# Performance work log

Hardware: AMD Instinct MI355X
Metric: run time of the kernel (lower is better)

The kernel has to match this reference:

```python
import jax, jax.numpy as jnp
import numpy as np

D_MODEL = 1024
D_STATE = 16
D_CONV = 4
EXPAND = 2
D_INNER = D_MODEL * EXPAND


def setup_inputs() -> dict:
    key = jax.random.key(0)
    ks = jax.random.split(key, 10)
    B, L = 2, 2048
    x = jax.random.normal(ks[0], (B, L, D_MODEL), jnp.float32)
    W_in = jax.random.normal(ks[1], (2 * D_INNER, D_MODEL), jnp.float32) * (1.0 / np.sqrt(D_MODEL))
    conv_w = jax.random.normal(ks[2], (D_INNER, 1, D_CONV), jnp.float32) * (1.0 / np.sqrt(D_CONV))
    conv_b = jax.random.normal(ks[3], (D_INNER,), jnp.float32) * 0.1
    W_x = jax.random.normal(ks[4], (2 * D_STATE + 1, D_INNER), jnp.float32) * (1.0 / np.sqrt(D_INNER))
    A_log = jnp.log(jnp.abs(jax.random.normal(ks[5], (D_INNER, D_STATE), jnp.float32)) + 1e-4)
    D_param = jnp.ones((D_INNER,), jnp.float32)
    W_dt = jax.random.normal(ks[6], (D_INNER, 1), jnp.float32)
    b_dt = jax.random.normal(ks[7], (D_INNER,), jnp.float32) * 0.1
    W_out = jax.random.normal(ks[8], (D_MODEL, D_INNER), jnp.float32) * (1.0 / np.sqrt(D_INNER))
    return {"x": x, "W_in": W_in, "conv_w": conv_w, "conv_b": conv_b, "W_x": W_x,
            "A_log": A_log, "D_param": D_param, "W_dt": W_dt, "b_dt": b_dt, "W_out": W_out}


def _forward(x, W_in, conv_w, conv_b, W_x, A_log, D_param, W_dt, b_dt, W_out):
    B, L, _ = x.shape
    xz = x @ W_in.T                                  # [B,L,2*d_inner]
    x_ssm, z = jnp.split(xz, 2, axis=-1)
    # causal depthwise conv: torch pads both sides d_conv-1 then truncates to L == left-pad only
    xc = jnp.transpose(x_ssm, (0, 2, 1))             # [B,d_inner,L]
    xc = jax.lax.conv_general_dilated(
        xc, conv_w, window_strides=(1,), padding=[(D_CONV - 1, 0)],
        feature_group_count=D_INNER, dimension_numbers=("NCH", "OIH", "NCH"))
    xc = xc + conv_b[None, :, None]
    x_ssm = jax.nn.silu(jnp.transpose(xc, (0, 2, 1)))  # [B,L,d_inner]
    proj = x_ssm @ W_x.T                              # [B,L,2*d_state+1]
    B_ssm = proj[..., :D_STATE]                       # [B,L,d_state]
    C_ssm = proj[..., D_STATE:2 * D_STATE]            # [B,L,d_state]
    dt = jax.nn.softplus(proj[..., -1:] * W_dt[:, 0] + b_dt)  # [B,L,d_inner]
    A = -jnp.exp(A_log)                               # [d_inner,d_state]

    def step(h, inp):
        dt_t, Bt, Ct, xt = inp                        # [B,d_inner],[B,n],[B,n],[B,d_inner]
        dA = jnp.exp(dt_t[..., None] * A)             # [B,d_inner,d_state]
        h = dA * h + (xt * dt_t)[..., None] * Bt[:, None, :]
        y = jnp.einsum("bdn,bn->bd", h, Ct)
        return h, y

    h0 = jnp.zeros((B, D_INNER, D_STATE), x.dtype)
    inputs = (jnp.transpose(dt, (1, 0, 2)), jnp.transpose(B_ssm, (1, 0, 2)),
              jnp.transpose(C_ssm, (1, 0, 2)), jnp.transpose(x_ssm, (1, 0, 2)))
    _, ys = jax.lax.scan(step, h0, inputs)            # ys: [L,B,d_inner]
    y = jnp.transpose(ys, (1, 0, 2)) + x_ssm * D_param
    y = y * jax.nn.silu(z)
    return y @ W_out.T


def reference(x, W_in, conv_w, conv_b, W_x, A_log, D_param, W_dt, b_dt, W_out):
    return _forward(x, W_in, conv_w, conv_b, W_x, A_log, D_param, W_dt, b_dt, W_out)
```

## Files before the change

kernel.cpp:

```cpp
#include <hip/hip_runtime.h>
#include <hip/hip_bf16.h>
#include <cstddef>

#define DMODEL 1024
#define DI     2048
#define DS     16
#define LSEQ   2048
#define BATCH  2
#define NC     128
#define TCH    (LSEQ / NC)

typedef __attribute__((ext_vector_type(8))) short short8;
typedef __attribute__((ext_vector_type(4))) float f32x4;
typedef __attribute__((ext_vector_type(2))) float f32x2;
typedef __attribute__((ext_vector_type(8))) unsigned short us8;

__device__ __forceinline__ unsigned short f2bf(float f) {
    unsigned int u = __float_as_uint(f);
    unsigned int r = (u + 0x7fff + ((u >> 16) & 1)) >> 16;
    return (unsigned short)r;
}
__device__ __forceinline__ float bf2f(unsigned short b) {
    return __uint_as_float(((unsigned int)b) << 16);
}

__device__ __forceinline__ float fexp2(float x) {
#if __has_builtin(__builtin_amdgcn_exp2f)
    return __builtin_amdgcn_exp2f(x);
#else
    return exp2f(x);
#endif
}
__device__ __forceinline__ float flog2(float x) {
#if __has_builtin(__builtin_amdgcn_logf)
    return __builtin_amdgcn_logf(x);
#else
    return log2f(x);
#endif
}

#define LOG2E 1.4426950408889634f
#define RLOG2E 0.6931471805599453f

__device__ __forceinline__ float softplus_f(float v) {
    return (v > 20.f) ? v : flog2(1.f + fexp2(v * LOG2E)) * RLOG2E;
}

__device__ __forceinline__ void gload_lds16(const void* g, void* l) {
    __builtin_amdgcn_global_load_lds(
        (const __attribute__((address_space(1))) unsigned int*)g,
        (__attribute__((address_space(3))) unsigned int*)l, 16, 0, 0);
}

__device__ __forceinline__ void cvt8_store(const float* __restrict__ in,
                                           unsigned short* __restrict__ out, int i) {
    const float4* p = reinterpret_cast<const float4*>(in) + (size_t)i * 2;
    float4 v0 = p[0], v1 = p[1];
    us8 o;
    o[0] = f2bf(v0.x); o[1] = f2bf(v0.y); o[2] = f2bf(v0.z); o[3] = f2bf(v0.w);
    o[4] = f2bf(v1.x); o[5] = f2bf(v1.y); o[6] = f2bf(v1.z); o[7] = f2bf(v1.w);
    *reinterpret_cast<us8*>(out + (size_t)i * 8) = o;
}

#define PREP_X   524288
#define PREP_WI  (PREP_X + 524288)
#define PREP_WO  (PREP_WI + 262144)
#define PREP_WX  (PREP_WO + 12288)
#define PREP_A   (PREP_WX + 32768)
__global__ void prep_all(const float* __restrict__ x, const float* __restrict__ W_in,
                         const float* __restrict__ W_out, const float* __restrict__ wx,
                         const float* __restrict__ A_log,
                         unsigned short* __restrict__ Xb, unsigned short* __restrict__ W_inb,
                         unsigned short* __restrict__ W_outb, unsigned short* __restrict__ Wxb48,
                         float* __restrict__ At2) {
    int i = blockIdx.x * 256 + threadIdx.x;
    if (i < PREP_X) {
        cvt8_store(x, Xb, i);
    } else if (i < PREP_WI) {
        cvt8_store(W_in, W_inb, i - PREP_X);
    } else if (i < PREP_WO) {
        cvt8_store(W_out, W_outb, i - PREP_WI);
    } else if (i < PREP_WX) {
        int j = i - PREP_WO;
        size_t o = (size_t)j * 8;
        int row = (int)(o >> 11);
        if (row < 33) cvt8_store(wx, Wxb48, j);
        else *reinterpret_cast<us8*>(Wxb48 + o) = (us8)0;
    } else if (i < PREP_A) {
        int j = i - PREP_WX;
        int n = j / DI, d = j % DI;
        At2[j] = -__expf(A_log[d * DS + n]) * LOG2E;
    }
}

#define NTK1 32
__global__ __launch_bounds__(512, 4)
void gemm1_2b(const unsigned short* __restrict__ A, const unsigned short* __restrict__ B,
              unsigned short* __restrict__ C) {
    __shared__ unsigned short As[2][128 * 32];
    __shared__ unsigned short Bs[2][256 * 32];

    const int tid = threadIdx.x;
    const int wid = tid >> 6, ln = tid & 63;
    const int wm = wid >> 2, wn = wid & 3;

    int wg = blockIdx.x;
    wg = (wg & 7) * 64 + (wg >> 3);
    const int m0 = (wg >> 4) * 128;
    const int n0 = (wg & 15) * 256;

    const int srow = tid >> 2;
    const int sun  = tid & 3;
    const int ksrc = ((sun ^ ((srow >> 1) & 3)) * 8);

    const int fr = ln & 15;
    const int fku = (ln >> 4);

    f32x4 acc[4][4] = {};

    #define STAGE1(kt, c)                                                                  \
        do {                                                                               \
            gload_lds16(A + (size_t)(m0 + srow) * 1024 + (kt) * 32 + ksrc,                 \
                        &As[c][srow * 32 + sun * 8]);                                      \
            gload_lds16(B + (size_t)(n0 + srow) * 1024 + (kt) * 32 + ksrc,                 \
                        &Bs[c][srow * 32 + sun * 8]);                                      \
            gload_lds16(B + (size_t)(n0 + 128 + srow) * 1024 + (kt) * 32 + ksrc,           \
                        &Bs[c][(128 + srow) * 32 + sun * 8]);                              \
        } while (0)

    STAGE1(0, 0);
    asm volatile("s_waitcnt vmcnt(0)" ::: "memory");
    __builtin_amdgcn_s_barrier();
    __builtin_amdgcn_sched_barrier(0);

    for (int kt = 0; kt < NTK1; ++kt) {
        const int c = kt & 1;
        if (kt + 1 < NTK1) STAGE1(kt + 1, c ^ 1);

        short8 af[4], bfr[4];
        #pragma unroll
        for (int i = 0; i < 4; ++i) {
            int r = wm * 64 + i * 16 + fr;
            int u = fku ^ ((r >> 1) & 3);
            af[i] = *reinterpret_cast<const short8*>(&As[c][r * 32 + u * 8]);
        }
        #pragma unroll
        for (int j = 0; j < 4; ++j) {
            int r = wn * 64 + j * 16 + fr;
            int u = fku ^ ((r >> 1) & 3);
            bfr[j] = *reinterpret_cast<const short8*>(&Bs[c][r * 32 + u * 8]);
        }
        __builtin_amdgcn_sched_barrier(0);
        __builtin_amdgcn_s_setprio(1);
        #pragma unroll
        for (int i = 0; i < 4; ++i)
            #pragma unroll
            for (int j = 0; j < 4; ++j)
                acc[i][j] = __builtin_amdgcn_mfma_f32_16x16x32_bf16(af[i], bfr[j], acc[i][j], 0, 0, 0);
        __builtin_amdgcn_s_setprio(0);
        __builtin_amdgcn_sched_barrier(0);

        if (kt + 1 < NTK1) asm volatile("s_waitcnt vmcnt(0)" ::: "memory");
        __builtin_amdgcn_s_barrier();
        __builtin_amdgcn_sched_barrier(0);
    }
    #undef STAGE1

    const int cr = (ln >> 4) * 4, cc = ln & 15;
    #pragma unroll
    for (int i = 0; i < 4; ++i) {
        int row = m0 + wm * 64 + i * 16 + cr;
        #pragma unroll
        for (int j = 0; j < 4; ++j) {
            int col = n0 + wn * 64 + j * 16 + cc;
            #pragma unroll
            for (int r = 0; r < 4; ++r)
                C[(size_t)(row + r) * 4096 + col] = f2bf(acc[i][j][r]);
        }
    }
}

#define NT3 64
__global__ __launch_bounds__(256, 2)
void gemm3_pipe(const unsigned short* __restrict__ A,
                const unsigned short* __restrict__ B,
                float* __restrict__ C) {
    __shared__ unsigned short As[4][128 * 32];
    __shared__ unsigned short Bs[4][64 * 32];

    const int tid = threadIdx.x;
    const int wid = tid >> 6, ln = tid & 63;
    const int wm = wid >> 1, wn = wid & 1;

    int wg = blockIdx.x;
    wg = (wg & 7) * 64 + (wg >> 3);
    const int m0 = (wg >> 4) * 128;
    const int n0 = (wg & 15) * 64;

    const int srow = tid >> 2;
    const int sun  = tid & 3;
    const int ksrc = ((sun ^ ((srow >> 1) & 3)) * 8);

    const int fr = ln & 15;
    const int fku = (ln >> 4);

    f32x4 acc[4][2] = {};

    #define STAGE3(kt)                                                                     \
        do {                                                                               \
            const int bq_ = (kt) & 3;                                                      \
            gload_lds16(A + (size_t)(m0 + srow) * 2048 + (kt) * 32 + ksrc,                 \
                        &As[bq_][srow * 32 + sun * 8]);                                    \
            gload_lds16(A + (size_t)(m0 + 64 + srow) * 2048 + (kt) * 32 + ksrc,            \
                        &As[bq_][(64 + srow) * 32 + sun * 8]);                             \
            gload_lds16(B + (size_t)(n0 + srow) * 2048 + (kt) * 32 + ksrc,                 \
                        &Bs[bq_][srow * 32 + sun * 8]);                                    \
        } while (0)

    STAGE3(0); STAGE3(1); STAGE3(2);
    asm volatile("s_waitcnt vmcnt(6)" ::: "memory");
    __builtin_amdgcn_s_barrier();
    __builtin_amdgcn_sched_barrier(0);

    for (int kt = 0; kt < NT3; ++kt) {
        const int bq = kt & 3;
        if (kt + 3 < NT3) STAGE3(kt + 3);

        short8 af[4], bfr[2];
        #pragma unroll
        for (int i = 0; i < 4; ++i) {
            int r = wm * 64 + i * 16 + fr;
            int u = fku ^ ((r >> 1) & 3);
            af[i] = *reinterpret_cast<const short8*>(&As[bq][r * 32 + u * 8]);
        }
        #pragma unroll
        for (int j = 0; j < 2; ++j) {
            int r = wn * 32 + j * 16 + fr;
            int u = fku ^ ((r >> 1) & 3);
            bfr[j] = *reinterpret_cast<const short8*>(&Bs[bq][r * 32 + u * 8]);
        }
        __builtin_amdgcn_sched_barrier(0);
        __builtin_amdgcn_s_setprio(1);
        #pragma unroll
        for (int i = 0; i < 4; ++i)
            #pragma unroll
            for (int j = 0; j < 2; ++j)
                acc[i][j] = __builtin_amdgcn_mfma_f32_16x16x32_bf16(af[i], bfr[j], acc[i][j], 0, 0, 0);
        __builtin_amdgcn_s_setprio(0);
        __builtin_amdgcn_sched_barrier(0);

        if (kt < NT3 - 3)       asm volatile("s_waitcnt vmcnt(6)" ::: "memory");
        else if (kt == NT3 - 3) asm volatile("s_waitcnt vmcnt(3)" ::: "memory");
        else if (kt == NT3 - 2) asm volatile("s_waitcnt vmcnt(0)" ::: "memory");
        __builtin_amdgcn_s_barrier();
        __builtin_amdgcn_sched_barrier(0);
    }
    #undef STAGE3

    const int cr = (ln >> 4) * 4, cc = ln & 15;
    #pragma unroll
    for (int i = 0; i < 4; ++i) {
        int row = m0 + wm * 64 + i * 16 + cr;
        #pragma unroll
        for (int j = 0; j < 2; ++j) {
            int col = n0 + wn * 32 + j * 16 + cc;
            #pragma unroll
            for (int r = 0; r < 4; ++r)
                C[(size_t)(row + r) * 1024 + col] = acc[i][j][r];
        }
    }
}

__global__ void conv_silu(const unsigned short* __restrict__ xzb, const float* __restrict__ cw,
                          const float* __restrict__ cb, unsigned short* __restrict__ xactb) {
    int i = blockIdx.x * 256 + threadIdx.x;
    if (i >= BATCH * LSEQ * DI / 8) return;
    int d0 = (i % (DI / 8)) * 8;
    int l  = (i / (DI / 8)) % LSEQ;
    int b  = i / ((DI / 8) * LSEQ);

    float4 w[8];
    #pragma unroll
    for (int j = 0; j < 8; ++j)
        w[j] = *reinterpret_cast<const float4*>(cw + (d0 + j) * 4);

    float acc[8];
    #pragma unroll
    for (int j = 0; j < 8; ++j) acc[j] = cb[d0 + j];

    #pragma unroll
    for (int t = 0; t < 4; ++t) {
        int ls = l - 3 + t;
        if (ls >= 0) {
            us8 v = *reinterpret_cast<const us8*>(xzb + (size_t)(b * LSEQ + ls) * 4096 + d0);
            #pragma unroll
            for (int j = 0; j < 8; ++j) {
                float wt = (t == 0) ? w[j].x : (t == 1) ? w[j].y : (t == 2) ? w[j].z : w[j].w;
                acc[j] += bf2f(v[j]) * wt;
            }
        }
    }
    us8 o;
    #pragma unroll
    for (int j = 0; j < 8; ++j) {
        float v = acc[j] / (1.f + __expf(-acc[j]));
        o[j] = f2bf(v);
    }
    *reinterpret_cast<us8*>(xactb + (size_t)i * 8) = o;
}

__global__ __launch_bounds__(256)
void gemm_proj_mfma(const unsigned short* __restrict__ Xb, const unsigned short* __restrict__ Wxb,
                    float* __restrict__ projp) {
    __shared__ unsigned short As[64 * 32];
    __shared__ unsigned short Bs[48 * 32];

    const int tid = threadIdx.x;
    const int wv = tid >> 6, ln = tid & 63;
    const int m0 = blockIdx.x * 64;
    const int kz = blockIdx.y;
    const int srow = tid >> 2, skoff = (tid & 3) * 8;
    const int fr = ln & 15, fk = (ln >> 4) * 8;

    f32x4 acc[3] = {};

    const int k0base = kz * 512;
    for (int k0 = k0base; k0 < k0base + 512; k0 += 32) {
        gload_lds16(Xb + (size_t)(m0 + srow) * DI + k0 + skoff, &As[wv * 512]);
        if (wv < 3)
            gload_lds16(Wxb + (size_t)srow * DI + k0 + skoff, &Bs[wv * 512]);
        __syncthreads();

        short8 af = *reinterpret_cast<const short8*>(&As[(wv * 16 + fr) * 32 + fk]);
        #pragma unroll
        for (int j = 0; j < 3; ++j) {
            short8 bf_ = *reinterpret_cast<const short8*>(&Bs[(j * 16 + fr) * 32 + fk]);
            acc[j] = __builtin_amdgcn_mfma_f32_16x16x32_bf16(af, bf_, acc[j], 0, 0, 0);
        }
        __syncthreads();
    }

    const int cr = (ln >> 4) * 4, cc = ln & 15;
    #pragma unroll
    for (int j = 0; j < 3; ++j) {
        int col = j * 16 + cc;
        if (col < 33) {
            #pragma unroll
            for (int r = 0; r < 4; ++r) {
                int row = m0 + wv * 16 + cr + r;
                projp[(size_t)row * 144 + kz * 36 + col] = acc[j][r];
            }
        }
    }
}

__global__ void proj_combine(const float* __restrict__ projp, float* __restrict__ proj) {
    int idx = blockIdx.x * 256 + threadIdx.x;
    if (idx >= BATCH * LSEQ * 33) return;
    int row = idx / 33, col = idx % 33;
    float s = 0.f;
    #pragma unroll
    for (int kz = 0; kz < 4; ++kz)
        s += projp[(size_t)row * 144 + kz * 36 + col];
    proj[(size_t)row * 36 + col] = s;
}

__global__ __launch_bounds__(256)
void scan_phase1(const unsigned short* __restrict__ xactb, const float* __restrict__ proj,
                 const float* __restrict__ At2, const float* __restrict__ W_dt,
                 const float* __restrict__ b_dt, const float* __restrict__ Dp,
                 unsigned short* __restrict__ Hend,
                 float* __restrict__ dtsum, unsigned short* __restrict__ yloc) {
    const int d = blockIdx.x * 256 + threadIdx.x;
    const int c = blockIdx.y;
    const int b = blockIdx.z;

    f32x2 A2[DS / 2], h2[DS / 2];
    #pragma unroll
    for (int p = 0; p < DS / 2; ++p) {
        A2[p] = (f32x2){At2[(2 * p) * DI + d], At2[(2 * p + 1) * DI + d]};
        h2[p] = (f32x2){0.f, 0.f};
    }
    const float wdt = W_dt[d], bdt = b_dt[d], Dv = Dp[d];
    float ssum = 0.f;

    const int l0 = c * TCH;
    #pragma unroll 2
    for (int l = l0; l < l0 + TCH; ++l) {
        const size_t row = (size_t)(b * LSEQ + l);
        const float* pr = proj + row * 36;
        float dt = softplus_f(pr[32] * wdt + bdt);
        ssum += dt;
        float x = bf2f(xactb[row * DI + d]);
        float xdt = x * dt;
        f32x2 xdt2 = (f32x2){xdt, xdt};
        f32x2 y2 = (f32x2){0.f, 0.f};
        #pragma unroll
        for (int p = 0; p < DS / 2; ++p) {
            f32x2 t = A2[p] * dt;
            f32x2 e2 = (f32x2){fexp2(t.x), fexp2(t.y)};
            h2[p] = e2 * h2[p] + xdt2 * (f32x2){pr[2 * p], pr[2 * p + 1]};
            y2 += h2[p] * (f32x2){pr[16 + 2 * p], pr[17 + 2 * p]};
        }
        yloc[row * DI + d] = f2bf(y2.x + y2.y + x * Dv);
    }
    size_t base = ((size_t)(b * NC + c) * DS) * DI + d;
    #pragma unroll
    for (int p = 0; p < DS / 2; ++p) {
        Hend[base + (size_t)(2 * p) * DI]     = f2bf(h2[p].x);
        Hend[base + (size_t)(2 * p + 1) * DI] = f2bf(h2[p].y);
    }
    dtsum[(size_t)(b * NC + c) * DI + d] = ssum;
}

__global__ void scan_phase2(unsigned short* __restrict__ H, const float* __restrict__ dtsum,
                            const float* __restrict__ At2) {
    int idx = blockIdx.x * 256 + threadIdx.x;
    int b = idx / (DS * DI);
    int r = idx % (DS * DI);
    int n = r / DI, d = r % DI;
    float A2 = At2[n * DI + d];
    float h = 0.f;
    #pragma unroll 4
    for (int c = 0; c < NC; ++c) {
        size_t off = ((size_t)(b * NC + c) * DS + n) * DI + d;
        float He = bf2f(H[off]);
        float P = fexp2(A2 * dtsum[(size_t)(b * NC + c) * DI + d]);
        H[off] = f2bf(h);
        h = P * h + He;
    }
}

__global__ __launch_bounds__(256)
void scan_phase3(const unsigned short* __restrict__ yloc,
                 const float* __restrict__ proj, const float* __restrict__ At2,
                 const float* __restrict__ W_dt, const float* __restrict__ b_dt,
                 const unsigned short* __restrict__ Hin,
                 const unsigned short* __restrict__ XZb,
                 unsigned short* __restrict__ YB2) {
    const int tid = threadIdx.x;
    const int d = blockIdx.x * 256 + tid;
    const int c = blockIdx.y;
    const int b = blockIdx.z;

    f32x2 A2[DS / 2], Hn2[DS / 2];
    size_t hbase = ((size_t)(b * NC + c) * DS) * DI + d;
    #pragma unroll
    for (int p = 0; p < DS / 2; ++p) {
        A2[p]  = (f32x2){At2[(2 * p) * DI + d], At2[(2 * p + 1) * DI + d]};
        Hn2[p] = (f32x2){bf2f(Hin[hbase + (size_t)(2 * p) * DI]),
                         bf2f(Hin[hbase + (size_t)(2 * p + 1) * DI])};
    }
    const float wdt = W_dt[d], bdt = b_dt[d];
    float S = 0.f;

    const int l0 = c * TCH;
    #pragma unroll 2
    for (int l = l0; l < l0 + TCH; ++l) {
        const size_t row = (size_t)(b * LSEQ + l);
        const float* pr = proj + row * 36;
        float dt = softplus_f(pr[32] * wdt + bdt);
        S += dt;
        float yl = bf2f(yloc[row * DI + d]);
        float z  = bf2f(XZb[row * 4096 + 2048 + d]);
        f32x2 corr2 = (f32x2){0.f, 0.f};
        #pragma unroll
        for (int p = 0; p < DS / 2; ++p) {
            f32x2 t = A2[p] * S;
            f32x2 e2 = (f32x2){fexp2(t.x), fexp2(t.y)};
            corr2 += (f32x2){pr[16 + 2 * p], pr[17 + 2 * p]} * e2 * Hn2[p];
        }
        float y = yl + corr2.x + corr2.y;
        float sz = z / (1.f + __expf(-z));
        YB2[row * DI + d] = f2bf(y * sz);
    }
}

extern "C" void kernel_launch(void* const* d_in, const int* in_sizes, int n_in,
                              void* d_out, int out_size, void* d_ws, size_t ws_size,
                              hipStream_t stream) {
    const float* x      = (const float*)d_in[0];
    const float* W_in   = (const float*)d_in[1];
    const float* conv_w = (const float*)d_in[2];
    const float* conv_b = (const float*)d_in[3];
    const float* W_x    = (const float*)d_in[4];
    const float* A_log  = (const float*)d_in[5];
    const float* Dp     = (const float*)d_in[6];
    const float* W_dt   = (const float*)d_in[7];
    const float* b_dt   = (const float*)d_in[8];
    const float* W_out  = (const float*)d_in[9];
    float* out = (float*)d_out;

    char* ws = (char*)d_ws;
    unsigned short* XZb   = (unsigned short*)(ws + 0);
    unsigned short* XACTB = (unsigned short*)(ws + 33554432);
    unsigned short* Xb    = (unsigned short*)(ws + 50331648);
    unsigned short* W_inb = (unsigned short*)(ws + 58720256);
    unsigned short* YB2   = (unsigned short*)(ws + 50331648);
    unsigned short* Hbuf  = (unsigned short*)(ws + 67108864);
    unsigned short* YLOC  = (unsigned short*)(ws + 83886080);
    float* PROJ  = (float*)(ws + 100663296);
    float* DTSUM = (float*)(ws + 101711872);
    float* PROJP = (float*)(ws + 103809024);
    float* Abuf  = (float*)(ws + 106954752);
    unsigned short* W_outb = (unsigned short*)(ws + 108003328);
    unsigned short* Wxb48  = (unsigned short*)(ws + 112197632);

    const int M = BATCH * LSEQ;

    prep_all<<<(PREP_A + 255) / 256, 256, 0, stream>>>(
        x, W_in, W_out, W_x, A_log, Xb, W_inb, W_outb, Wxb48, Abuf);

    gemm1_2b<<<512, 512, 0, stream>>>(Xb, W_inb, XZb);

    conv_silu<<<BATCH * LSEQ * DI / 8 / 256, 256, 0, stream>>>(XZb, conv_w, conv_b, XACTB);

    gemm_proj_mfma<<<dim3(M / 64, 4), 256, 0, stream>>>(XACTB, Wxb48, PROJP);
    proj_combine<<<(M * 33 + 255) / 256, 256, 0, stream>>>(PROJP, PROJ);

    scan_phase1<<<dim3(DI / 256, NC, BATCH), 256, 0, stream>>>(
        XACTB, PROJ, Abuf, W_dt, b_dt, Dp, Hbuf, DTSUM, YLOC);
    scan_phase2<<<BATCH * DS * DI / 256, 256, 0, stream>>>(Hbuf, DTSUM, Abuf);
    scan_phase3<<<dim3(DI / 256, NC, BATCH), 256, 0, stream>>>(
        YLOC, PROJ, Abuf, W_dt, b_dt, Hbuf, XZb, YB2);

    gemm3_pipe<<<512, 256, 0, stream>>>(YB2, W_outb, out);
}
```

Before: 202.1 us.

## Fuse causal conv+SiLU into x_proj GEMM and fold split-K reduction into scans

Removes the standalone conv_silu kernel by computing the depthwise causal conv and SiLU inside the x_proj MFMA GEMM. Each block stages a 67-row halo tile of the xz activations in LDS, builds the bf16 A fragment directly, and also writes the activations out for the scan. Removes proj_combine by having scan phases 1 and 3 sum the four split-K partials into shared memory per chunk. This saves two launches and an activation round trip. In exchange the global-to-LDS staging is now synchronous, and the partial-sum reduction is repeated across the d-blocks.

```diff
diff --git a/kernel.cpp b/kernel.cpp
--- a/kernel.cpp
+++ b/kernel.cpp
@@ -271,48 +271,12 @@
     }
 }
 
-__global__ void conv_silu(const unsigned short* __restrict__ xzb, const float* __restrict__ cw,
-                          const float* __restrict__ cb, unsigned short* __restrict__ xactb) {
-    int i = blockIdx.x * 256 + threadIdx.x;
-    if (i >= BATCH * LSEQ * DI / 8) return;
-    int d0 = (i % (DI / 8)) * 8;
-    int l  = (i / (DI / 8)) % LSEQ;
-    int b  = i / ((DI / 8) * LSEQ);
-
-    float4 w[8];
-    #pragma unroll
-    for (int j = 0; j < 8; ++j)
-        w[j] = *reinterpret_cast<const float4*>(cw + (d0 + j) * 4);
-
-    float acc[8];
-    #pragma unroll
-    for (int j = 0; j < 8; ++j) acc[j] = cb[d0 + j];
-
-    #pragma unroll
-    for (int t = 0; t < 4; ++t) {
-        int ls = l - 3 + t;
-        if (ls >= 0) {
-            us8 v = *reinterpret_cast<const us8*>(xzb + (size_t)(b * LSEQ + ls) * 4096 + d0);
-            #pragma unroll
-            for (int j = 0; j < 8; ++j) {
-                float wt = (t == 0) ? w[j].x : (t == 1) ? w[j].y : (t == 2) ? w[j].z : w[j].w;
-                acc[j] += bf2f(v[j]) * wt;
-            }
-        }
-    }
-    us8 o;
-    #pragma unroll
-    for (int j = 0; j < 8; ++j) {
-        float v = acc[j] / (1.f + __expf(-acc[j]));
-        o[j] = f2bf(v);
-    }
-    *reinterpret_cast<us8*>(xactb + (size_t)i * 8) = o;
-}
-
+#define RAWS 40
 __global__ __launch_bounds__(256)
-void gemm_proj_mfma(const unsigned short* __restrict__ Xb, const unsigned short* __restrict__ Wxb,
-                    float* __restrict__ projp) {
-    __shared__ unsigned short As[64 * 32];
+void gemm_proj_conv(const unsigned short* __restrict__ XZb, const unsigned short* __restrict__ Wxb,
+                    const float* __restrict__ cw, const float* __restrict__ cb,
+                    float* __restrict__ projp, unsigned short* __restrict__ xactb) {
+    __shared__ unsigned short raw[67 * RAWS];
     __shared__ unsigned short Bs[48 * 32];
 
     const int tid = threadIdx.x;
@@ -320,21 +284,52 @@
     const int m0 = blockIdx.x * 64;
     const int kz = blockIdx.y;
     const int srow = tid >> 2, skoff = (tid & 3) * 8;
-    const int fr = ln & 15, fk = (ln >> 4) * 8;
+    const int fr = ln & 15;
+    const int lhat = wv * 16 + fr;
+    const int d0 = (ln >> 4) * 8;
+
+    const bool mstart = ((m0 & 2047) == 0);
+    const int colbase = kz * 512;
 
     f32x4 acc[3] = {};
 
-    const int k0base = kz * 512;
-    for (int k0 = k0base; k0 < k0base + 512; k0 += 32) {
-        gload_lds16(Xb + (size_t)(m0 + srow) * DI + k0 + skoff, &As[wv * 512]);
+    for (int k0 = 0; k0 < 512; k0 += 32) {
+        for (int j = tid; j < 268; j += 256) {
+            int i = j >> 2, slot = j & 3;
+            us8 v;
+            if (mstart && i < 3) {
+                v = (us8)0;
+            } else {
+                v = *reinterpret_cast<const us8*>(
+                    XZb + (size_t)(m0 - 3 + i) * 4096 + colbase + k0 + slot * 8);
+            }
+            *reinterpret_cast<us8*>(&raw[i * RAWS + slot * 8]) = v;
+        }
         if (wv < 3)
-            gload_lds16(Wxb + (size_t)srow * DI + k0 + skoff, &Bs[wv * 512]);
+            gload_lds16(Wxb + (size_t)srow * 2048 + colbase + k0 + skoff, &Bs[wv * 512]);
         __syncthreads();
 
-        short8 af = *reinterpret_cast<const short8*>(&As[(wv * 16 + fr) * 32 + fk]);
+        short8 af;
+        us8 ax;
+        #pragma unroll
+        for (int e = 0; e < 8; ++e) {
+            int dg = colbase + k0 + d0 + e;
+            float a = cb[dg];
+            float4 w = *reinterpret_cast<const float4*>(cw + dg * 4);
+            a += bf2f(raw[(lhat + 0) * RAWS + d0 + e]) * w.x;
+            a += bf2f(raw[(lhat + 1) * RAWS + d0 + e]) * w.y;
+            a += bf2f(raw[(lhat + 2) * RAWS + d0 + e]) * w.z;
+            a += bf2f(raw[(lhat + 3) * RAWS + d0 + e]) * w.w;
+            float v = a / (1.f + __expf(-a));
+            unsigned short bfv = f2bf(v);
+            ((unsigned short*)&af)[e] = (short)bfv;
+            ax[e] = bfv;
+        }
+        *reinterpret_cast<us8*>(xactb + (size_t)(m0 + lhat) * 2048 + colbase + k0 + d0) = ax;
+
         #pragma unroll
         for (int j = 0; j < 3; ++j) {
-            short8 bf_ = *reinterpret_cast<const short8*>(&Bs[(j * 16 + fr) * 32 + fk]);
+            short8 bf_ = *reinterpret_cast<const short8*>(&Bs[(j * 16 + fr) * 32 + d0]);
             acc[j] = __builtin_amdgcn_mfma_f32_16x16x32_bf16(af, bf_, acc[j], 0, 0, 0);
         }
         __syncthreads();
@@ -354,26 +349,25 @@
     }
 }
 
-__global__ void proj_combine(const float* __restrict__ projp, float* __restrict__ proj) {
-    int idx = blockIdx.x * 256 + threadIdx.x;
-    if (idx >= BATCH * LSEQ * 33) return;
-    int row = idx / 33, col = idx % 33;
-    float s = 0.f;
-    #pragma unroll
-    for (int kz = 0; kz < 4; ++kz)
-        s += projp[(size_t)row * 144 + kz * 36 + col];
-    proj[(size_t)row * 36 + col] = s;
-}
-
 __global__ __launch_bounds__(256)
-void scan_phase1(const unsigned short* __restrict__ xactb, const float* __restrict__ proj,
+void scan_phase1(const unsigned short* __restrict__ xactb, const float* __restrict__ projp,
                  const float* __restrict__ At2, const float* __restrict__ W_dt,
                  const float* __restrict__ b_dt, const float* __restrict__ Dp,
                  unsigned short* __restrict__ Hend,
                  float* __restrict__ dtsum, unsigned short* __restrict__ yloc) {
+    __shared__ float prS[TCH][34];
+
     const int d = blockIdx.x * 256 + threadIdx.x;
     const int c = blockIdx.y;
     const int b = blockIdx.z;
+    const size_t r0 = (size_t)(b * LSEQ + c * TCH);
+
+    for (int idx = threadIdx.x; idx < TCH * 33; idx += 256) {
+        int rl = idx / 33, col = idx % 33;
+        const float* pp = projp + (r0 + rl) * 144 + col;
+        prS[rl][col] = ((pp[0] + pp[36]) + pp[72]) + pp[108];
+    }
+    __syncthreads();
 
     f32x2 A2[DS / 2], h2[DS / 2];
     #pragma unroll
@@ -384,11 +378,10 @@
     const float wdt = W_dt[d], bdt = b_dt[d], Dv = Dp[d];
     float ssum = 0.f;
 
-    const int l0 = c * TCH;
     #pragma unroll 2
-    for (int l = l0; l < l0 + TCH; ++l) {
-        const size_t row = (size_t)(b * LSEQ + l);
-        const float* pr = proj + row * 36;
+    for (int rl = 0; rl < TCH; ++rl) {
+        const size_t row = r0 + rl;
+        const float* pr = prS[rl];
         float dt = softplus_f(pr[32] * wdt + bdt);
         ssum += dt;
         float x = bf2f(xactb[row * DI + d]);
@@ -433,15 +426,25 @@
 
 __global__ __launch_bounds__(256)
 void scan_phase3(const unsigned short* __restrict__ yloc,
-                 const float* __restrict__ proj, const float* __restrict__ At2,
+                 const float* __restrict__ projp, const float* __restrict__ At2,
                  const float* __restrict__ W_dt, const float* __restrict__ b_dt,
                  const unsigned short* __restrict__ Hin,
                  const unsigned short* __restrict__ XZb,
                  unsigned short* __restrict__ YB2) {
+    __shared__ float prS[TCH][34];
+
     const int tid = threadIdx.x;
     const int d = blockIdx.x * 256 + tid;
     const int c = blockIdx.y;
     const int b = blockIdx.z;
+    const size_t r0 = (size_t)(b * LSEQ + c * TCH);
+
+    for (int idx = tid; idx < TCH * 33; idx += 256) {
+        int rl = idx / 33, col = idx % 33;
+        const float* pp = projp + (r0 + rl) * 144 + col;
+        prS[rl][col] = ((pp[0] + pp[36]) + pp[72]) + pp[108];
+    }
+    __syncthreads();
 
     f32x2 A2[DS / 2], Hn2[DS / 2];
     size_t hbase = ((size_t)(b * NC + c) * DS) * DI + d;
@@ -454,11 +457,10 @@
     const float wdt = W_dt[d], bdt = b_dt[d];
     float S = 0.f;
 
-    const int l0 = c * TCH;
     #pragma unroll 2
-    for (int l = l0; l < l0 + TCH; ++l) {
-        const size_t row = (size_t)(b * LSEQ + l);
-        const float* pr = proj + row * 36;
+    for (int rl = 0; rl < TCH; ++rl) {
+        const size_t row = r0 + rl;
+        const float* pr = prS[rl];
         float dt = softplus_f(pr[32] * wdt + bdt);
         S += dt;
         float yl = bf2f(yloc[row * DI + d]);
@@ -499,7 +501,6 @@
     unsigned short* YB2   = (unsigned short*)(ws + 50331648);
     unsigned short* Hbuf  = (unsigned short*)(ws + 67108864);
     unsigned short* YLOC  = (unsigned short*)(ws + 83886080);
-    float* PROJ  = (float*)(ws + 100663296);
     float* DTSUM = (float*)(ws + 101711872);
     float* PROJP = (float*)(ws + 103809024);
     float* Abuf  = (float*)(ws + 106954752);
@@ -513,16 +514,14 @@
 
     gemm1_2b<<<512, 512, 0, stream>>>(Xb, W_inb, XZb);
 
-    conv_silu<<<BATCH * LSEQ * DI / 8 / 256, 256, 0, stream>>>(XZb, conv_w, conv_b, XACTB);
-
-    gemm_proj_mfma<<<dim3(M / 64, 4), 256, 0, stream>>>(XACTB, Wxb48, PROJP);
-    proj_combine<<<(M * 33 + 255) / 256, 256, 0, stream>>>(PROJP, PROJ);
+    gemm_proj_conv<<<dim3(M / 64, 4), 256, 0, stream>>>(
+        XZb, Wxb48, conv_w, conv_b, PROJP, XACTB);
 
     scan_phase1<<<dim3(DI / 256, NC, BATCH), 256, 0, stream>>>(
-        XACTB, PROJ, Abuf, W_dt, b_dt, Dp, Hbuf, DTSUM, YLOC);
+        XACTB, PROJP, Abuf, W_dt, b_dt, Dp, Hbuf, DTSUM, YLOC);
     scan_phase2<<<BATCH * DS * DI / 256, 256, 0, stream>>>(Hbuf, DTSUM, Abuf);
     scan_phase3<<<dim3(DI / 256, NC, BATCH), 256, 0, stream>>>(
-        YLOC, PROJ, Abuf, W_dt, b_dt, Hbuf, XZb, YB2);
+        YLOC, PROJP, Abuf, W_dt, b_dt, Hbuf, XZb, YB2);
 
     gemm3_pipe<<<512, 256, 0, stream>>>(YB2, W_outb, out);
 }
```

Result: faster. 194.1 us (-4.0%).
